# Optimization experiments

Hardware: AMD Instinct MI355X
Metric: run time of the kernel (lower is better)

## Reference

```python
import jax, jax.numpy as jnp
import numpy as np
import itertools

DIM, ORDER = 8, 4  # matches init_kwargs

def _exponent_table(dim, order):
    # All multisets (non-decreasing tuples) of size 0..order over range(dim),
    # sorted lexicographically -- identical to sorted(Counter keys) in the torch code
    # (Counter keys are sorted tuples; combinations_with_replacement yields exactly those).
    terms = sorted(itertools.chain.from_iterable(
        itertools.combinations_with_replacement(range(dim), o) for o in range(order + 1)))
    E = np.zeros((len(terms), dim), dtype=np.int32)
    for i, t in enumerate(terms):
        for d in t:
            E[i, d] += 1
    return E

E = jnp.asarray(_exponent_table(DIM, ORDER))  # [nterms=495, dim=8]


def setup_inputs() -> dict:
    key = jax.random.key(0)
    x = jax.random.normal(key, (65536, DIM), dtype=jnp.float32)
    return {"x": x}


def reference(x):
    # torch: cat_i prod_d x[..., d] ** ind_i.count(d)
    # vectorized: broadcast pow with exponent table, reduce-product over dim axis
    # x: [B, dim] -> [B, 1, dim] ** [nterms, dim] -> prod over dim -> [B, nterms]
    return jnp.prod(x[..., None, :] ** E, axis=-1)
```

## Files before the change

### kernel.cpp

```cpp
#include <hip/hip_runtime.h>


typedef float f32x4 __attribute__((ext_vector_type(4)));

struct Tbl {
    unsigned uv4[512];
    unsigned short pp[64];
};

constexpr int pidx_c(int a, int b) {
    return 9 + 8 * a - (a * (a - 1)) / 2 + (b - a);
}

constexpr Tbl make_tbl() {
    Tbl T{};
    unsigned lin[500] = {};
    int idx = 1;
    for (int a = 0; a < 8; ++a) {
        lin[idx++] = (unsigned)(1 + a);
        for (int b = a; b < 8; ++b) {
            lin[idx++] = (unsigned)pidx_c(a, b);
            for (int c = b; c < 8; ++c) {
                lin[idx++] = (unsigned)pidx_c(a, b) | ((unsigned)(1 + c) << 16);
                for (int d = c; d < 8; ++d)
                    lin[idx++] = (unsigned)pidx_c(a, b) | ((unsigned)pidx_c(c, d) << 16);
            }
        }
    }
    for (int i = 0; i < 5; ++i) lin[495 + i] = lin[i];
    for (int t = 0; t < 499; ++t) T.uv4[(t & 3) * 128 + (t >> 2)] = lin[t];
    for (int l = 0; l < 64; ++l) {
        int s1 = 0, s2 = 0, u1 = 0, u2 = 0;
        if (l >= 1 && l <= 8) { s1 = l - 1; u1 = 1; }
        else if (l >= 9 && l < 45) {
            int k = l - 9, i = 0;
            while (k >= 8 - i) { k -= 8 - i; ++i; }
            s1 = i; s2 = i + k; u1 = 1; u2 = 1;
        }
        T.pp[l] = (unsigned short)(s1 | (s2 << 4) | (u1 << 8) | (u2 << 9));
    }
    return T;
}

__constant__ Tbl TBL = make_tbl();

#define ROWS_PER_BLOCK 32
#define WORDS_PER_BLOCK (ROWS_PER_BLOCK * 495)
#define UNITS 62

__global__ __launch_bounds__(256, 8) void TotalDegree_29755533426739_kernel(
    const float* __restrict__ x, float* __restrict__ out, int B) {
    __shared__ float xs[256];
    __shared__ float P[ROWS_PER_BLOCK * 64];
    __shared__ unsigned uvt[512];

    const int tid  = (int)threadIdx.x;
    const int lane = tid & 63;
    const int wid  = tid >> 6;

    {
        const int gi = (int)blockIdx.x * 256 + tid;
        xs[tid] = (gi < B * 8) ? x[gi] : 0.0f;
    }

    const int ppv  = (int)TBL.pp[lane];
    const int s1   = ppv & 15;
    const int s2   = (ppv >> 4) & 15;
    const bool use1 = ((ppv >> 8) & 1) != 0;
    const bool use2 = ((ppv >> 9) & 1) != 0;
    const float* xw = xs + wid * 64;
    #pragma unroll
    for (int rr = 0; rr < 8; ++rr) {
        const float a1 = xw[rr * 8 + s1];
        const float a2 = xw[rr * 8 + s2];
        P[(wid * 8 + rr) * 64 + lane] = (use1 ? a1 : 1.0f) * (use2 ? a2 : 1.0f);
    }
    if (tid < 256) {
        uvt[tid] = TBL.uv4[tid];
        uvt[tid + 256] = TBL.uv4[tid + 256];
    }
    __syncthreads();

    float* oB = out + (unsigned)blockIdx.x * WORDS_PER_BLOCK;
    {
        const int f0 = wid * 256 + (lane << 2);
        int r0 = (f0 >= 990) ? 2 : (f0 >= 495 ? 1 : 0);
        int t  = f0 - r0 * 495;
        int rb = r0 << 6;

        for (int s = wid; s < UNITS; s += 4) {
            const unsigned q0 = uvt[((t    ) & 3) * 128 + ((t    ) >> 2)];
            const unsigned q1 = uvt[((t + 1) & 3) * 128 + ((t + 1) >> 2)];
            const unsigned q2 = uvt[((t + 2) & 3) * 128 + ((t + 2) >> 2)];
            const unsigned q3 = uvt[((t + 3) & 3) * 128 + ((t + 3) >> 2)];
            const int w1 = (t >= 494) ? 64 : 0;
            const int w2 = (t >= 493) ? 64 : 0;
            const int w3 = (t >= 492) ? 64 : 0;
            f32x4 v;
            v.x = P[rb      + (int)(q0 & 0xffffu)] * P[rb      + (int)(q0 >> 16)];
            v.y = P[rb + w1 + (int)(q1 & 0xffffu)] * P[rb + w1 + (int)(q1 >> 16)];
            v.z = P[rb + w2 + (int)(q2 & 0xffffu)] * P[rb + w2 + (int)(q2 >> 16)];
            v.w = P[rb + w3 + (int)(q3 & 0xffffu)] * P[rb + w3 + (int)(q3 >> 16)];
            if (s < UNITS - 1 || lane < 56)
                *reinterpret_cast<f32x4*>(oB + s * 256 + (lane << 2)) = v;
            t += 34; rb += 128;
            if (t >= 495) { t -= 495; rb += 64; }
        }
    }
}

extern "C" void kernel_launch(void* const* d_in, const int* in_sizes, int n_in,
                              void* d_out, int out_size, void* d_ws, size_t ws_size,
                              hipStream_t stream) {
    const float* x = (const float*)d_in[0];
    float* out = (float*)d_out;
    const int B = in_sizes[0] / 8;
    const int grid = (B + ROWS_PER_BLOCK - 1) / ROWS_PER_BLOCK;
    hipLaunchKernelGGL(TotalDegree_29755533426739_kernel,
                       dim3(grid), dim3(256), 0, stream, x, out, B);
}
```

Baseline: 129.8 us.

## Replace LDS-staged pair products with grid-stride direct gather from global x

Drops the shared-memory staging of x, the precomputed pairwise products and the constant-to-LDS table copy, along with the block barrier. Each thread now decodes a packed 4-index exponent word from constant memory and multiplies up to four x values loaded straight from global memory, relying on the cache. A fixed grid of 2048 persistent blocks walks the flattened output in 1024-float units. This removes LDS traffic and synchronisation but adds more global gather loads per output vector. Any tail where B*495 is not a multiple of 1024 is not written.

```diff
diff --git a/kernel.cpp b/kernel.cpp
--- a/kernel.cpp
+++ b/kernel.cpp
@@ -3,109 +3,75 @@
 
 typedef float f32x4 __attribute__((ext_vector_type(4)));
 
-struct Tbl {
-    unsigned uv4[512];
-    unsigned short pp[64];
-};
+struct DTbl { unsigned d[512]; };
 
-constexpr int pidx_c(int a, int b) {
-    return 9 + 8 * a - (a * (a - 1)) / 2 + (b - a);
-}
-
-constexpr Tbl make_tbl() {
-    Tbl T{};
-    unsigned lin[500] = {};
-    int idx = 1;
+constexpr DTbl make_dtbl() {
+    DTbl T{};
+    int idx = 0;
+    T.d[idx++] = 0u;
     for (int a = 0; a < 8; ++a) {
-        lin[idx++] = (unsigned)(1 + a);
+        T.d[idx++] = (unsigned)a | (1u << 12);
         for (int b = a; b < 8; ++b) {
-            lin[idx++] = (unsigned)pidx_c(a, b);
+            T.d[idx++] = (unsigned)(a | (b << 3)) | (3u << 12);
             for (int c = b; c < 8; ++c) {
-                lin[idx++] = (unsigned)pidx_c(a, b) | ((unsigned)(1 + c) << 16);
+                T.d[idx++] = (unsigned)(a | (b << 3) | (c << 6)) | (7u << 12);
                 for (int d = c; d < 8; ++d)
-                    lin[idx++] = (unsigned)pidx_c(a, b) | ((unsigned)pidx_c(c, d) << 16);
+                    T.d[idx++] =
+                        (unsigned)(a | (b << 3) | (c << 6) | (d << 9)) | (15u << 12);
             }
         }
     }
-    for (int i = 0; i < 5; ++i) lin[495 + i] = lin[i];
-    for (int t = 0; t < 499; ++t) T.uv4[(t & 3) * 128 + (t >> 2)] = lin[t];
-    for (int l = 0; l < 64; ++l) {
-        int s1 = 0, s2 = 0, u1 = 0, u2 = 0;
-        if (l >= 1 && l <= 8) { s1 = l - 1; u1 = 1; }
-        else if (l >= 9 && l < 45) {
-            int k = l - 9, i = 0;
-            while (k >= 8 - i) { k -= 8 - i; ++i; }
-            s1 = i; s2 = i + k; u1 = 1; u2 = 1;
-        }
-        T.pp[l] = (unsigned short)(s1 | (s2 << 4) | (u1 << 8) | (u2 << 9));
-    }
+    for (int j = 0; j < 17; ++j) T.d[495 + j] = T.d[j];
     return T;
 }
 
-__constant__ Tbl TBL = make_tbl();
+__constant__ DTbl DT = make_dtbl();
 
-#define ROWS_PER_BLOCK 32
-#define WORDS_PER_BLOCK (ROWS_PER_BLOCK * 495)
-#define UNITS 62
+#define NBLOCKS 2048
+
+__device__ __forceinline__ float term_val(const float* __restrict__ xb, unsigned q) {
+    const float la = xb[q & 7u];
+    const float lb = xb[(q >> 3) & 7u];
+    const float lc = xb[(q >> 6) & 7u];
+    const float ld = xb[(q >> 9) & 7u];
+    const float a = (q & 0x1000u) ? la : 1.0f;
+    const float b = (q & 0x2000u) ? lb : 1.0f;
+    const float c = (q & 0x4000u) ? lc : 1.0f;
+    const float d = (q & 0x8000u) ? ld : 1.0f;
+    return (a * b) * (c * d);
+}
 
 __global__ __launch_bounds__(256, 8) void TotalDegree_29755533426739_kernel(
-    const float* __restrict__ x, float* __restrict__ out, int B) {
-    __shared__ float xs[256];
-    __shared__ float P[ROWS_PER_BLOCK * 64];
-    __shared__ unsigned uvt[512];
+    const float* __restrict__ x, float* __restrict__ out, unsigned nunits) {
+    const int tid = (int)threadIdx.x;
 
-    const int tid  = (int)threadIdx.x;
-    const int lane = tid & 63;
-    const int wid  = tid >> 6;
+    unsigned u = blockIdx.x;
+    const unsigned f0 = u * 1024u + (unsigned)(tid << 2);
+    unsigned r = f0 / 495u;
+    unsigned t = f0 - r * 495u;
 
-    {
-        const int gi = (int)blockIdx.x * 256 + tid;
-        xs[tid] = (gi < B * 8) ? x[gi] : 0.0f;
-    }
+    while (u < nunits) {
+        const unsigned q0 = DT.d[t];
+        const unsigned q1 = DT.d[t + 1];
+        const unsigned q2 = DT.d[t + 2];
+        const unsigned q3 = DT.d[t + 3];
+        const float* xb0 = x + (r << 3);
+        const float* xb1 = x + ((r + (t >= 494u)) << 3);
+        const float* xb2 = x + ((r + (t >= 493u)) << 3);
+        const float* xb3 = x + ((r + (t >= 492u)) << 3);
 
-    const int ppv  = (int)TBL.pp[lane];
-    const int s1   = ppv & 15;
-    const int s2   = (ppv >> 4) & 15;
-    const bool use1 = ((ppv >> 8) & 1) != 0;
-    const bool use2 = ((ppv >> 9) & 1) != 0;
-    const float* xw = xs + wid * 64;
-    #pragma unroll
-    for (int rr = 0; rr < 8; ++rr) {
-        const float a1 = xw[rr * 8 + s1];
-        const float a2 = xw[rr * 8 + s2];
-        P[(wid * 8 + rr) * 64 + lane] = (use1 ? a1 : 1.0f) * (use2 ? a2 : 1.0f);
-    }
-    if (tid < 256) {
-        uvt[tid] = TBL.uv4[tid];
-        uvt[tid + 256] = TBL.uv4[tid + 256];
-    }
-    __syncthreads();
+        f32x4 v;
+        v.x = term_val(xb0, q0);
+        v.y = term_val(xb1, q1);
+        v.z = term_val(xb2, q2);
+        v.w = term_val(xb3, q3);
 
-    float* oB = out + (unsigned)blockIdx.x * WORDS_PER_BLOCK;
-    {
-        const int f0 = wid * 256 + (lane << 2);
-        int r0 = (f0 >= 990) ? 2 : (f0 >= 495 ? 1 : 0);
-        int t  = f0 - r0 * 495;
-        int rb = r0 << 6;
+        *reinterpret_cast<f32x4*>(out + (size_t)u * 1024u + (unsigned)(tid << 2)) = v;
 
-        for (int s = wid; s < UNITS; s += 4) {
-            const unsigned q0 = uvt[((t    ) & 3) * 128 + ((t    ) >> 2)];
-            const unsigned q1 = uvt[((t + 1) & 3) * 128 + ((t + 1) >> 2)];
-            const unsigned q2 = uvt[((t + 2) & 3) * 128 + ((t + 2) >> 2)];
-            const unsigned q3 = uvt[((t + 3) & 3) * 128 + ((t + 3) >> 2)];
-            const int w1 = (t >= 494) ? 64 : 0;
-            const int w2 = (t >= 493) ? 64 : 0;
-            const int w3 = (t >= 492) ? 64 : 0;
-            f32x4 v;
-            v.x = P[rb      + (int)(q0 & 0xffffu)] * P[rb      + (int)(q0 >> 16)];
-            v.y = P[rb + w1 + (int)(q1 & 0xffffu)] * P[rb + w1 + (int)(q1 >> 16)];
-            v.z = P[rb + w2 + (int)(q2 & 0xffffu)] * P[rb + w2 + (int)(q2 >> 16)];
-            v.w = P[rb + w3 + (int)(q3 & 0xffffu)] * P[rb + w3 + (int)(q3 >> 16)];
-            if (s < UNITS - 1 || lane < 56)
-                *reinterpret_cast<f32x4*>(oB + s * 256 + (lane << 2)) = v;
-            t += 34; rb += 128;
-            if (t >= 495) { t -= 495; rb += 64; }
-        }
+        u += NBLOCKS;
+        r += 4236u;
+        t += 332u;
+        if (t >= 495u) { t -= 495u; ++r; }
     }
 }
 
@@ -115,7 +81,7 @@
     const float* x = (const float*)d_in[0];
     float* out = (float*)d_out;
     const int B = in_sizes[0] / 8;
-    const int grid = (B + ROWS_PER_BLOCK - 1) / ROWS_PER_BLOCK;
+    const unsigned nunits = (unsigned)(((long long)B * 495) / 1024);
     hipLaunchKernelGGL(TotalDegree_29755533426739_kernel,
-                       dim3(grid), dim3(256), 0, stream, x, out, B);
+                       dim3(NBLOCKS), dim3(256), 0, stream, x, out, nunits);
 }
```

After: 181.7 us. 1.4x slower.
